# Performance work log

Hardware: AMD Instinct MI355X
Metric: run time of the kernel (lower is better)

Reference implementation:

```python
import jax, jax.numpy as jnp
import numpy as np

B, C, A, H, W = 8, 64, 32, 64, 64  # batch, input_nf, atten_nf, height, width

def setup_inputs() -> dict:
    key = jax.random.key(0)
    k = jax.random.split(key, 5)
    scale = 1.0 / np.sqrt(C)
    return {
        "x":  jax.random.normal(k[0], (B, C, H, W), dtype=jnp.float32),
        "Wg": jax.random.uniform(k[1], (A, C), jnp.float32, -scale, scale),  # 1x1 conv kernel
        "bg": jax.random.uniform(k[2], (A,),   jnp.float32, -scale, scale),
        "Wh": jax.random.uniform(k[3], (A, C), jnp.float32, -scale, scale),
        "bh": jax.random.uniform(k[4], (A,),   jnp.float32, -scale, scale),
    }

def reference(x, Wg, bg, Wh, bh):
    b, c, h, w = x.shape
    n = h * w
    xf = x.reshape(b, c, n)                               # [B, C, N]
    g = jnp.einsum('ac,bcn->ban', Wg, xf) + bg[None, :, None]  # 1x1 conv == GEMM
    hq = jnp.einsum('ac,bcn->ban', Wh, xf) + bh[None, :, None]
    scores = jnp.einsum('ban,bam->bnm', g, hq)            # [B, N, N]
    alpha = jax.nn.softmax(scores, axis=2)
    r = jnp.einsum('bnm,bcm->bcn', alpha, xf)             # alpha @ x^T, back to [B,C,N]
    r = r.reshape(b, c, h, w)
    r = r + x  # is_residual=True
    return (jax.nn.relu(r), alpha)
```

## Files before the change

### kernel.cpp

```cpp
#include <hip/hip_runtime.h>
#include <hip/hip_bf16.h>
#include <math.h>

#define NB 8
#define NC 64
#define NA 32
#define NN 4096
#define NWAVE 8

typedef __attribute__((ext_vector_type(8))) short bf16x8;
typedef __attribute__((ext_vector_type(4))) float f32x4;

__device__ inline ushort f2bf(float f) {
  union { float f; unsigned u; } v; v.f = f;
  unsigned r = v.u + 0x7fffu + ((v.u >> 16) & 1u);
  return (ushort)(r >> 16);
}

__device__ inline bf16x8 pack8(const f32x4 a, const f32x4 b) {
  union { ushort us[8]; bf16x8 v; } u;
#pragma unroll
  for (int i = 0; i < 4; ++i) { u.us[i] = f2bf(a[i]); u.us[4 + i] = f2bf(b[i]); }
  return u.v;
}

__global__ __launch_bounds__(256) void prep_kernel(
    const float* __restrict__ x, const float* __restrict__ Wg, const float* __restrict__ bg,
    const float* __restrict__ Wh, const float* __restrict__ bh,
    ushort* __restrict__ gT, ushort* __restrict__ hqT, ushort* __restrict__ xfb)
{
  __shared__ float wg_s[NA * NC];
  __shared__ float wh_s[NA * NC];
  const int t = threadIdx.x;
  for (int i = t; i < NA * NC; i += 256) { wg_s[i] = Wg[i]; wh_s[i] = Wh[i]; }
  __syncthreads();

  const int gid = blockIdx.x * 256 + t;
  const int b = gid >> 12;
  const int n = gid & (NN - 1);
  const float* xb = x + (size_t)b * NC * NN + n;

  float accg[NA], acch[NA];
#pragma unroll
  for (int a = 0; a < NA; ++a) { accg[a] = 0.f; acch[a] = 0.f; }

  for (int c4 = 0; c4 < NC / 4; ++c4) {
    const float xv0 = xb[(size_t)(c4 * 4 + 0) * NN];
    const float xv1 = xb[(size_t)(c4 * 4 + 1) * NN];
    const float xv2 = xb[(size_t)(c4 * 4 + 2) * NN];
    const float xv3 = xb[(size_t)(c4 * 4 + 3) * NN];
    const size_t xo = ((size_t)b * NC + c4 * 4) * NN + n;
    xfb[xo]          = f2bf(xv0);
    xfb[xo + NN]     = f2bf(xv1);
    xfb[xo + 2 * NN] = f2bf(xv2);
    xfb[xo + 3 * NN] = f2bf(xv3);
#pragma unroll
    for (int a = 0; a < NA; ++a) {
      const float4 wg4 = *(const float4*)&wg_s[a * NC + c4 * 4];
      const float4 wh4 = *(const float4*)&wh_s[a * NC + c4 * 4];
      accg[a] += wg4.x * xv0 + wg4.y * xv1 + wg4.z * xv2 + wg4.w * xv3;
      acch[a] += wh4.x * xv0 + wh4.y * xv1 + wh4.z * xv2 + wh4.w * xv3;
    }
  }

  const float LOG2E = 1.44269504088896340736f;
  ushort og[NA], oh[NA];
#pragma unroll
  for (int a = 0; a < NA; ++a) {
    og[a] = f2bf((accg[a] + bg[a]) * LOG2E);
    oh[a] = f2bf(acch[a] + bh[a]);
  }
  const size_t o = ((size_t)b * NN + n) * NA;
#pragma unroll
  for (int k = 0; k < 4; ++k) {
    uint4 vg, vh;
    vg.x = (uint)og[k*8+0] | ((uint)og[k*8+1] << 16);
    vg.y = (uint)og[k*8+2] | ((uint)og[k*8+3] << 16);
    vg.z = (uint)og[k*8+4] | ((uint)og[k*8+5] << 16);
    vg.w = (uint)og[k*8+6] | ((uint)og[k*8+7] << 16);
    vh.x = (uint)oh[k*8+0] | ((uint)oh[k*8+1] << 16);
    vh.y = (uint)oh[k*8+2] | ((uint)oh[k*8+3] << 16);
    vh.z = (uint)oh[k*8+4] | ((uint)oh[k*8+5] << 16);
    vh.w = (uint)oh[k*8+6] | ((uint)oh[k*8+7] << 16);
    *(uint4*)(gT  + o + k * 8) = vg;
    *(uint4*)(hqT + o + k * 8) = vh;
  }
}

__global__ __launch_bounds__(512, 4) void attn_kernel(
    const ushort* __restrict__ gT, const ushort* __restrict__ hqT,
    const ushort* __restrict__ xfb, const float* __restrict__ x,
    float* __restrict__ outp, float* __restrict__ alpha)
{
  __shared__ float plds[NWAVE][32][32];
  __shared__ float rtile[32][65];
  __shared__ float Lp[NWAVE][32];

  const int tid = threadIdx.x;
  const int l  = tid & 63;
  const int w  = tid >> 6;
  const int lm = l & 15;
  const int lh = l >> 4;
  const int b  = blockIdx.x >> 7;
  const int n0 = (blockIdx.x & 127) << 5;
  const int mbase = w << 9;

  const ushort* gB = gT  + (size_t)b * NN * NA;
  const ushort* hB = hqT + (size_t)b * NN * NA;
  const ushort* xB = xfb + (size_t)b * NC * NN;

  bf16x8 gb0 = *(const bf16x8*)(gB + (size_t)(n0 + lm) * NA + lh * 8);
  bf16x8 gb1 = *(const bf16x8*)(gB + (size_t)(n0 + 16 + lm) * NA + lh * 8);
  bf16x8 ha0 = *(const bf16x8*)(hB + (size_t)(mbase + lm) * NA + lh * 8);
  bf16x8 ha1 = *(const bf16x8*)(hB + (size_t)(mbase + 16 + lm) * NA + lh * 8);

  float* rflat = &rtile[0][0];
  for (int i = tid; i < 32 * 65; i += 512) rflat[i] = 0.f;

  const f32x4 zz = {0.f, 0.f, 0.f, 0.f};

  float sume0 = 0.f, sume1 = 0.f;
  for (int mc = 0; mc < 16; ++mc) {
    const int m1 = mbase + (((mc + 1) & 15) << 5);
    const bf16x8 na0 = *(const bf16x8*)(hB + (size_t)(m1 + lm) * NA + lh * 8);
    const bf16x8 na1 = *(const bf16x8*)(hB + (size_t)(m1 + 16 + lm) * NA + lh * 8);

    const f32x4 s00 = __builtin_amdgcn_mfma_f32_16x16x32_bf16(ha0, gb0, zz, 0, 0, 0);
    const f32x4 s10 = __builtin_amdgcn_mfma_f32_16x16x32_bf16(ha1, gb0, zz, 0, 0, 0);
    const f32x4 s01 = __builtin_amdgcn_mfma_f32_16x16x32_bf16(ha0, gb1, zz, 0, 0, 0);
    const f32x4 s11 = __builtin_amdgcn_mfma_f32_16x16x32_bf16(ha1, gb1, zz, 0, 0, 0);
#pragma unroll
    for (int r = 0; r < 4; ++r) {
      sume0 += exp2f(s00[r]) + exp2f(s10[r]);
      sume1 += exp2f(s01[r]) + exp2f(s11[r]);
    }
    ha0 = na0; ha1 = na1;
  }
  sume0 += __shfl_xor(sume0, 16); sume0 += __shfl_xor(sume0, 32);
  sume1 += __shfl_xor(sume1, 16); sume1 += __shfl_xor(sume1, 32);
  if (l < 16) { Lp[w][l] = sume0; Lp[w][16 + l] = sume1; }
  __syncthreads();

  float Ls0 = 0.f, Ls1 = 0.f;
#pragma unroll
  for (int ww = 0; ww < NWAVE; ++ww) { Ls0 += Lp[ww][lm]; Ls1 += Lp[ww][16 + lm]; }
  const float Linv0 = 1.0f / Ls0;
  const float Linv1 = 1.0f / Ls1;

  f32x4 racc[2][4];
#pragma unroll
  for (int gi = 0; gi < 2; ++gi)
#pragma unroll
    for (int ci = 0; ci < 4; ++ci) racc[gi][ci] = zz;

  float* aB = alpha + ((size_t)b * NN + n0) * NN;
  const int k7   = lm & 7;
  const int nrow = l >> 3;
  const int uu   = l & 7;

  for (int mc = 0; mc < 16; ++mc) {
    const int m0 = mbase + (mc << 5);
    const int m1 = mbase + (((mc + 1) & 15) << 5);
    const bf16x8 na0 = *(const bf16x8*)(hB + (size_t)(m1 + lm) * NA + lh * 8);
    const bf16x8 na1 = *(const bf16x8*)(hB + (size_t)(m1 + 16 + lm) * NA + lh * 8);

    const f32x4 s00 = __builtin_amdgcn_mfma_f32_16x16x32_bf16(ha0, gb0, zz, 0, 0, 0);
    const f32x4 s10 = __builtin_amdgcn_mfma_f32_16x16x32_bf16(ha1, gb0, zz, 0, 0, 0);
    const f32x4 s01 = __builtin_amdgcn_mfma_f32_16x16x32_bf16(ha0, gb1, zz, 0, 0, 0);
    const f32x4 s11 = __builtin_amdgcn_mfma_f32_16x16x32_bf16(ha1, gb1, zz, 0, 0, 0);

    f32x4 p00, p10, p01, p11;
#pragma unroll
    for (int r = 0; r < 4; ++r) {
      p00[r] = exp2f(s00[r]) * Linv0;
      p10[r] = exp2f(s10[r]) * Linv0;
      p01[r] = exp2f(s01[r]) * Linv1;
      p11[r] = exp2f(s11[r]) * Linv1;
    }

    *(f32x4*)&plds[w][lm]     [((lh    ) ^ k7) << 2] = p00;
    *(f32x4*)&plds[w][lm]     [((lh + 4) ^ k7) << 2] = p10;
    *(f32x4*)&plds[w][16 + lm][((lh    ) ^ k7) << 2] = p01;
    *(f32x4*)&plds[w][16 + lm][((lh + 4) ^ k7) << 2] = p11;

#pragma unroll
    for (int j = 0; j < 4; ++j) {
      const int row = j * 8 + nrow;
      const f32x4 pv = *(const f32x4*)&plds[w][row][(uu ^ (row & 7)) << 2];
      __builtin_nontemporal_store(pv, (f32x4*)(aB + (size_t)row * NN + m0 + uu * 4));
    }

    const f32x4 q00 = *(const f32x4*)&plds[w][lm]     [((2 * lh    ) ^ k7) << 2];
    const f32x4 q01 = *(const f32x4*)&plds[w][lm]     [((2 * lh + 1) ^ k7) << 2];
    const f32x4 q10 = *(const f32x4*)&plds[w][16 + lm][((2 * lh    ) ^ k7) << 2];
    const f32x4 q11 = *(const f32x4*)&plds[w][16 + lm][((2 * lh + 1) ^ k7) << 2];
    const bf16x8 pa0 = pack8(q00, q01);
    const bf16x8 pa1 = pack8(q10, q11);

#pragma unroll
    for (int ci = 0; ci < 4; ++ci) {
      const bf16x8 xv = *(const bf16x8*)(xB + (size_t)(ci * 16 + lm) * NN + m0 + lh * 8);
      racc[0][ci] = __builtin_amdgcn_mfma_f32_16x16x32_bf16(pa0, xv, racc[0][ci], 0, 0, 0);
      racc[1][ci] = __builtin_amdgcn_mfma_f32_16x16x32_bf16(pa1, xv, racc[1][ci], 0, 0, 0);
    }
    ha0 = na0; ha1 = na1;
  }

#pragma unroll
  for (int gi = 0; gi < 2; ++gi)
#pragma unroll
    for (int ci = 0; ci < 4; ++ci)
#pragma unroll
      for (int r = 0; r < 4; ++r)
        atomicAdd(&rtile[gi * 16 + lh * 4 + r][ci * 16 + lm], racc[gi][ci][r]);
  __syncthreads();

  const int c  = tid >> 3;
  const int j4 = (tid & 7) << 2;
  f32x4 v;
#pragma unroll
  for (int k = 0; k < 4; ++k) v[k] = rtile[j4 + k][c];
  const size_t oo = ((size_t)b * NC + c) * NN + n0 + j4;
  const f32x4 xr = *(const f32x4*)(x + oo);
#pragma unroll
  for (int k = 0; k < 4; ++k) {
    const float t = v[k] + xr[k];
    v[k] = t > 0.f ? t : 0.f;
  }
  __builtin_nontemporal_store(v, (f32x4*)(outp + oo));
}

extern "C" void kernel_launch(void* const* d_in, const int* in_sizes, int n_in,
                              void* d_out, int out_size, void* d_ws, size_t ws_size,
                              hipStream_t stream) {
  const float* x  = (const float*)d_in[0];
  const float* Wg = (const float*)d_in[1];
  const float* bg = (const float*)d_in[2];
  const float* Wh = (const float*)d_in[3];
  const float* bh = (const float*)d_in[4];

  float* outp  = (float*)d_out;
  float* alpha = outp + (size_t)NB * NC * NN;

  ushort* gT  = (ushort*)d_ws;
  ushort* hqT = gT + (size_t)NB * NN * NA;
  ushort* xfb = hqT + (size_t)NB * NN * NA;

  prep_kernel<<<NB * NN / 256, 256, 0, stream>>>(x, Wg, bg, Wh, bh, gT, hqT, xfb);
  attn_kernel<<<NB * (NN / 32), 512, 0, stream>>>(gT, hqT, xfb, x, outp, alpha);
}
```

Baseline: 227.3 us.

## Tile x into 16-column blocks, feed P@X MFMA from registers, remap blocks

The bf16 copy of x is now stored tiled as [n/16][C][16], so each 16-position chunk of all channels is contiguous. In the attention kernel the probability tiles are converted straight from registers with packed bf16 conversion and fed to 16x16x16 MFMAs, which removes the LDS read-back and software pack step before the P@X product. Workgroups are also remapped so consecutive block IDs land on different batches, which likely spreads L2/XCD traffic. The trade-off is twice as many smaller MFMA instructions, plus inline asm whose availability depends on the target.

```diff
diff --git a/kernel.cpp b/kernel.cpp
--- a/kernel.cpp
+++ b/kernel.cpp
@@ -9,7 +9,18 @@
 #define NWAVE 8
 
 typedef __attribute__((ext_vector_type(8))) short bf16x8;
+typedef __attribute__((ext_vector_type(4))) short bf16x4;
 typedef __attribute__((ext_vector_type(4))) float f32x4;
+
+#if __has_builtin(__builtin_amdgcn_mfma_f32_16x16x16bf16_1k)
+  #define HAVE_MFMA16 1
+  #define MFMA16(A,B,C) __builtin_amdgcn_mfma_f32_16x16x16bf16_1k(A,B,C,0,0,0)
+#elif __has_builtin(__builtin_amdgcn_mfma_f32_16x16x16_bf16)
+  #define HAVE_MFMA16 1
+  #define MFMA16(A,B,C) __builtin_amdgcn_mfma_f32_16x16x16_bf16(A,B,C,0,0,0)
+#else
+  #define HAVE_MFMA16 0
+#endif
 
 __device__ inline ushort f2bf(float f) {
   union { float f; unsigned u; } v; v.f = f;
@@ -24,10 +35,19 @@
   return u.v;
 }
 
+#if HAVE_MFMA16
+__device__ inline bf16x4 pk4(const f32x4 p) {
+  union { uint u[2]; bf16x4 v; } t;
+  asm("v_cvt_pk_bf16_f32 %0, %1, %2" : "=v"(t.u[0]) : "v"(p[0]), "v"(p[1]));
+  asm("v_cvt_pk_bf16_f32 %0, %1, %2" : "=v"(t.u[1]) : "v"(p[2]), "v"(p[3]));
+  return t.v;
+}
+#endif
+
 __global__ __launch_bounds__(256) void prep_kernel(
     const float* __restrict__ x, const float* __restrict__ Wg, const float* __restrict__ bg,
     const float* __restrict__ Wh, const float* __restrict__ bh,
-    ushort* __restrict__ gT, ushort* __restrict__ hqT, ushort* __restrict__ xfb)
+    ushort* __restrict__ gT, ushort* __restrict__ hqT, ushort* __restrict__ xfb2)
 {
   __shared__ float wg_s[NA * NC];
   __shared__ float wh_s[NA * NC];
@@ -39,6 +59,7 @@
   const int b = gid >> 12;
   const int n = gid & (NN - 1);
   const float* xb = x + (size_t)b * NC * NN + n;
+  const size_t x2base = (size_t)b * NC * NN + (size_t)(n >> 4) * (NC * 16) + (n & 15);
 
   float accg[NA], acch[NA];
 #pragma unroll
@@ -49,11 +70,10 @@
     const float xv1 = xb[(size_t)(c4 * 4 + 1) * NN];
     const float xv2 = xb[(size_t)(c4 * 4 + 2) * NN];
     const float xv3 = xb[(size_t)(c4 * 4 + 3) * NN];
-    const size_t xo = ((size_t)b * NC + c4 * 4) * NN + n;
-    xfb[xo]          = f2bf(xv0);
-    xfb[xo + NN]     = f2bf(xv1);
-    xfb[xo + 2 * NN] = f2bf(xv2);
-    xfb[xo + 3 * NN] = f2bf(xv3);
+    xfb2[x2base + (size_t)(c4 * 4 + 0) * 16] = f2bf(xv0);
+    xfb2[x2base + (size_t)(c4 * 4 + 1) * 16] = f2bf(xv1);
+    xfb2[x2base + (size_t)(c4 * 4 + 2) * 16] = f2bf(xv2);
+    xfb2[x2base + (size_t)(c4 * 4 + 3) * 16] = f2bf(xv3);
 #pragma unroll
     for (int a = 0; a < NA; ++a) {
       const float4 wg4 = *(const float4*)&wg_s[a * NC + c4 * 4];
@@ -89,7 +109,7 @@
 
 __global__ __launch_bounds__(512, 4) void attn_kernel(
     const ushort* __restrict__ gT, const ushort* __restrict__ hqT,
-    const ushort* __restrict__ xfb, const float* __restrict__ x,
+    const ushort* __restrict__ xfb2, const float* __restrict__ x,
     float* __restrict__ outp, float* __restrict__ alpha)
 {
   __shared__ float plds[NWAVE][32][32];
@@ -101,16 +121,18 @@
   const int w  = tid >> 6;
   const int lm = l & 15;
   const int lh = l >> 4;
-  const int b  = blockIdx.x >> 7;
-  const int n0 = (blockIdx.x & 127) << 5;
-  const int mbase = w << 9;
-
-  const ushort* gB = gT  + (size_t)b * NN * NA;
-  const ushort* hB = hqT + (size_t)b * NN * NA;
-  const ushort* xB = xfb + (size_t)b * NC * NN;
+
+  const int wgid = (blockIdx.x & 7) * 128 + (blockIdx.x >> 3);
+  const int b  = wgid >> 7;
+  const int n0 = (wgid & 127) << 5;
+
+  const ushort* gB  = gT   + (size_t)b * NN * NA;
+  const ushort* hB  = hqT  + (size_t)b * NN * NA;
+  const ushort* xB2 = xfb2 + (size_t)b * NC * NN;
 
   bf16x8 gb0 = *(const bf16x8*)(gB + (size_t)(n0 + lm) * NA + lh * 8);
   bf16x8 gb1 = *(const bf16x8*)(gB + (size_t)(n0 + 16 + lm) * NA + lh * 8);
+  const int mbase = w << 9;
   bf16x8 ha0 = *(const bf16x8*)(hB + (size_t)(mbase + lm) * NA + lh * 8);
   bf16x8 ha1 = *(const bf16x8*)(hB + (size_t)(mbase + 16 + lm) * NA + lh * 8);
 
@@ -190,19 +212,35 @@
       __builtin_nontemporal_store(pv, (f32x4*)(aB + (size_t)row * NN + m0 + uu * 4));
     }
 
+    const int t0 = m0 >> 4;
+#if HAVE_MFMA16
+    const bf16x4 A00 = pk4(p00);
+    const bf16x4 A01 = pk4(p10);
+    const bf16x4 A10 = pk4(p01);
+    const bf16x4 A11 = pk4(p11);
+#pragma unroll
+    for (int ci = 0; ci < 4; ++ci) {
+      const bf16x4 xv0 = *(const bf16x4*)(xB2 + (size_t)t0       * (NC * 16) + (ci * 16 + lm) * 16 + lh * 4);
+      const bf16x4 xv1 = *(const bf16x4*)(xB2 + (size_t)(t0 + 1) * (NC * 16) + (ci * 16 + lm) * 16 + lh * 4);
+      racc[0][ci] = MFMA16(A00, xv0, racc[0][ci]);
+      racc[0][ci] = MFMA16(A01, xv1, racc[0][ci]);
+      racc[1][ci] = MFMA16(A10, xv0, racc[1][ci]);
+      racc[1][ci] = MFMA16(A11, xv1, racc[1][ci]);
+    }
+#else
     const f32x4 q00 = *(const f32x4*)&plds[w][lm]     [((2 * lh    ) ^ k7) << 2];
     const f32x4 q01 = *(const f32x4*)&plds[w][lm]     [((2 * lh + 1) ^ k7) << 2];
     const f32x4 q10 = *(const f32x4*)&plds[w][16 + lm][((2 * lh    ) ^ k7) << 2];
     const f32x4 q11 = *(const f32x4*)&plds[w][16 + lm][((2 * lh + 1) ^ k7) << 2];
     const bf16x8 pa0 = pack8(q00, q01);
     const bf16x8 pa1 = pack8(q10, q11);
-
 #pragma unroll
     for (int ci = 0; ci < 4; ++ci) {
-      const bf16x8 xv = *(const bf16x8*)(xB + (size_t)(ci * 16 + lm) * NN + m0 + lh * 8);
+      const bf16x8 xv = *(const bf16x8*)(xB2 + (size_t)(t0 + (lh >> 1)) * (NC * 16) + (ci * 16 + lm) * 16 + (lh & 1) * 8);
       racc[0][ci] = __builtin_amdgcn_mfma_f32_16x16x32_bf16(pa0, xv, racc[0][ci], 0, 0, 0);
       racc[1][ci] = __builtin_amdgcn_mfma_f32_16x16x32_bf16(pa1, xv, racc[1][ci], 0, 0, 0);
     }
+#endif
     ha0 = na0; ha1 = na1;
   }
 
@@ -242,10 +280,10 @@
   float* outp  = (float*)d_out;
   float* alpha = outp + (size_t)NB * NC * NN;
 
-  ushort* gT  = (ushort*)d_ws;
-  ushort* hqT = gT + (size_t)NB * NN * NA;
-  ushort* xfb = hqT + (size_t)NB * NN * NA;
-
-  prep_kernel<<<NB * NN / 256, 256, 0, stream>>>(x, Wg, bg, Wh, bh, gT, hqT, xfb);
-  attn_kernel<<<NB * (NN / 32), 512, 0, stream>>>(gT, hqT, xfb, x, outp, alpha);
-}
+  ushort* gT   = (ushort*)d_ws;
+  ushort* hqT  = gT + (size_t)NB * NN * NA;
+  ushort* xfb2 = hqT + (size_t)NB * NN * NA;
+
+  prep_kernel<<<NB * NN / 256, 256, 0, stream>>>(x, Wg, bg, Wh, bh, gT, hqT, xfb2);
+  attn_kernel<<<NB * (NN / 32), 512, 0, stream>>>(gT, hqT, xfb2, x, outp, alpha);
+}
```

Result: faster. 213.0 us (-6.3%).
